# Kernel tuning notes

Hardware: AMD Instinct MI355X
Metric: run time of the kernel (lower is better)

## Reference

```python
import jax, jax.numpy as jnp
import numpy as np


def setup_inputs() -> dict:
    key = jax.random.key(0)
    k_u, k_a, k_b, k_c, k_d = jax.random.split(key, 5)
    B, T, Din, Dout, S = 16, 4096, 256, 256, 256
    return {
        "u": jax.random.normal(k_u, (B, T, Din), dtype=jnp.float32),
        "a_raw": jnp.zeros((S,), dtype=jnp.float32),
        "b": jax.random.normal(k_b, (S, Din), dtype=jnp.float32) * 0.1,
        "c": jax.random.normal(k_c, (Dout, S), dtype=jnp.float32) * 0.1,
        "d": jax.random.normal(k_d, (Dout, Din), dtype=jnp.float32) * 0.1,
    }


def reference(u, a_raw, b, c, d):
    # u: (B, T, Din) -> y: (B, T, Dout)
    # Recurrence: x_t = a * x_{t-1} + b @ u_t ;  y_t = c @ x_t + d @ u_t
    a = jnp.tanh(a_raw)                                  # (S,)
    Bu = jnp.einsum('btd,sd->bts', u, b)                 # input projection, (B,T,S)

    def step(x, bu_t):
        x = x * a + bu_t                                 # diagonal state update
        return x, x

    x0 = jnp.zeros((u.shape[0], a.shape[0]), dtype=u.dtype)
    _, xs = jax.lax.scan(step, x0, jnp.swapaxes(Bu, 0, 1))  # xs: (T,B,S)
    xs = jnp.swapaxes(xs, 0, 1)                              # (B,T,S)

    y = jnp.einsum('bts,os->bto', xs, c) + jnp.einsum('bti,oi->bto', u, d)
    return y  # dropout(p=0.0) is identity
```

## Files before the change

kernel.cpp:

```cpp
#include <hip/hip_runtime.h>

#define DEV __device__ __forceinline__

typedef unsigned short u16;
typedef __attribute__((ext_vector_type(8))) __bf16 bf16x8;
typedef __attribute__((ext_vector_type(4))) float f32x4;
typedef __attribute__((ext_vector_type(8))) unsigned short u16x8;

DEV u16 f2bf(float f) {
  unsigned u = __builtin_bit_cast(unsigned, f);
  u += 0x7fffu + ((u >> 16) & 1u);
  return (u16)(u >> 16);
}
DEV float bf2f(u16 h) {
  unsigned u = ((unsigned)h) << 16;
  return __builtin_bit_cast(float, u);
}

DEV void gl_lds16(const void* gp, void* lp) {
  __builtin_amdgcn_global_load_lds(
      (__attribute__((address_space(1))) void*)(void*)gp,
      (__attribute__((address_space(3))) void*)lp, 16, 0, 0);
}

__global__ __launch_bounds__(256) void prep_k(const float* __restrict__ a_raw,
                                              const float* __restrict__ b,
                                              const float* __restrict__ c,
                                              const float* __restrict__ d,
                                              float* __restrict__ af,
                                              u16* __restrict__ bw,
                                              u16* __restrict__ cw,
                                              u16* __restrict__ dw) {
  int i = blockIdx.x * 256 + threadIdx.x;
  if (i < 256) af[i] = tanhf(a_raw[i]);
  bw[i] = f2bf(b[i]);
  cw[i] = f2bf(c[i]);
  dw[i] = f2bf(d[i]);
}

__global__ __launch_bounds__(256) void convu_k(const float* __restrict__ u,
                                               u16* __restrict__ ub) {
  size_t i = ((size_t)blockIdx.x * 256 + threadIdx.x) * 8;
  float4 v0 = *reinterpret_cast<const float4*>(u + i);
  float4 v1 = *reinterpret_cast<const float4*>(u + i + 4);
  u16x8 o;
  o[0] = f2bf(v0.x); o[1] = f2bf(v0.y); o[2] = f2bf(v0.z); o[3] = f2bf(v0.w);
  o[4] = f2bf(v1.x); o[5] = f2bf(v1.y); o[6] = f2bf(v1.z); o[7] = f2bf(v1.w);
  *reinterpret_cast<u16x8*>(ub + i) = o;
}

__global__ __launch_bounds__(256) void gemm1_k(const u16* __restrict__ ubf,
                                               const u16* __restrict__ bw,
                                               const float* __restrict__ af,
                                               u16* __restrict__ bu,
                                               float* __restrict__ carry4) {
  __shared__ u16 As[2 * 128 * 64];
  __shared__ u16 Bs[2 * 128 * 64];
  const int tid = threadIdx.x;
  const int lane = tid & 63;
  const int wid = tid >> 6;
  const int wm = wid >> 1, wn = wid & 1;
  const int panel = blockIdx.x;
  const size_t row0 = (size_t)blockIdx.y * 128;
  const int col0 = panel * 128;

  const int rstg = tid >> 3;
  const int c16 = tid & 7;

  const f32x4 zero = {0.f, 0.f, 0.f, 0.f};
  f32x4 acc[4][4];
#pragma unroll
  for (int i = 0; i < 4; ++i)
#pragma unroll
    for (int j = 0; j < 4; ++j) acc[i][j] = zero;

#define G1_STAGE(ktv, bufv)                                                  \
  {                                                                          \
    const int kb_ = (ktv) * 64;                                              \
    _Pragma("unroll") for (int j = 0; j < 4; ++j) {                          \
      int row = j * 32 + rstg;                                               \
      int sc = c16 ^ (row & 7);                                              \
      gl_lds16(ubf + (row0 + row) * 256 + kb_ + sc * 8,                      \
               (char*)As + (bufv)*16384 + j * 4096 + wid * 1024);            \
      gl_lds16(bw + (size_t)(col0 + row) * 256 + kb_ + sc * 8,               \
               (char*)Bs + (bufv)*16384 + j * 4096 + wid * 1024);            \
    }                                                                        \
  }

  G1_STAGE(0, 0);
  __syncthreads();

#pragma unroll
  for (int kt = 0; kt < 4; ++kt) {
    const int cur = kt & 1;
    if (kt < 3) G1_STAGE(kt + 1, cur ^ 1);
    const u16* Ab = As + cur * 8192;
    const u16* Bb = Bs + cur * 8192;
#pragma unroll
    for (int kk = 0; kk < 2; ++kk) {
      const int ks = kk * 4 + (lane >> 4);
      bf16x8 afr[4], bfr[4];
#pragma unroll
      for (int mi = 0; mi < 4; ++mi) {
        int ar = wm * 64 + mi * 16 + (lane & 15);
        afr[mi] = *reinterpret_cast<const bf16x8*>(&Ab[ar * 64 + (ks ^ (ar & 7)) * 8]);
      }
#pragma unroll
      for (int ni = 0; ni < 4; ++ni) {
        int br = wn * 64 + ni * 16 + (lane & 15);
        bfr[ni] = *reinterpret_cast<const bf16x8*>(&Bb[br * 64 + (ks ^ (br & 7)) * 8]);
      }
#pragma unroll
      for (int mi = 0; mi < 4; ++mi)
#pragma unroll
        for (int ni = 0; ni < 4; ++ni)
          acc[mi][ni] = __builtin_amdgcn_mfma_f32_16x16x32_bf16(
              afr[mi], bfr[ni], acc[mi][ni], 0, 0, 0);
    }
    if (kt < 3) __syncthreads();
  }

  const size_t t2 = (size_t)blockIdx.y * 2 + wm;
#pragma unroll
  for (int mi = 0; mi < 4; ++mi) {
    int rbase = mi * 16 + (lane >> 4) * 4;
#pragma unroll
    for (int ni = 0; ni < 4; ++ni) {
      int col = col0 + wn * 64 + ni * 16 + (lane & 15);
      int colpart = (col >> 6) * 4096 + (col & 7);
      int sl = (col >> 3) & 7;
#pragma unroll
      for (int q = 0; q < 4; ++q) {
        int r = rbase + q;
        bu[t2 * 16384 + colpart + r * 64 + ((sl ^ (r & 7)) * 8)] = f2bf(acc[mi][ni][q]);
      }
    }
  }

  {
    const int tb = (lane >> 4) * 4;
#pragma unroll
    for (int ni = 0; ni < 4; ++ni) {
      int col = col0 + wn * 64 + ni * 16 + (lane & 15);
      float a = af[col];
      float c2 = a * a, c4 = c2 * c2, c8 = c4 * c4, a12 = c8 * c4;
      float base = (tb == 0) ? a12 : (tb == 4) ? c8 : (tb == 8) ? c4 : 1.0f;
#pragma unroll
      for (int mi = 0; mi < 4; ++mi) {
        float p = base, sq = 0.f;
#pragma unroll
        for (int q = 3; q >= 0; --q) {
          sq = fmaf(p, acc[mi][ni][q], sq);
          if (q) p *= a;
        }
        sq += __shfl_xor(sq, 16, 64);
        sq += __shfl_xor(sq, 32, 64);
        if ((lane >> 4) == 0) carry4[t2 * 1024 + mi * 256 + col] = sq;
      }
    }
  }
}

__global__ __launch_bounds__(256) void scan2_k(const float* __restrict__ carry4,
                                               const float* __restrict__ af,
                                               float* __restrict__ initb4) {
  int b = blockIdx.x;
  int s = threadIdx.x;
  float a = af[s];
  float a16 = a * a; a16 = a16 * a16; a16 = a16 * a16; a16 = a16 * a16;
  float x = 0.f;
  size_t base = (size_t)b * 64 * 1024 + s;
  float c0 = carry4[base], c1 = carry4[base + 256],
        c2 = carry4[base + 512], c3 = carry4[base + 768];
  for (int k = 0; k < 64; ++k) {
    size_t idx = base + (size_t)k * 1024;
    float n0 = 0.f, n1 = 0.f, n2 = 0.f, n3 = 0.f;
    if (k < 63) {
      size_t nx = idx + 1024;
      n0 = carry4[nx]; n1 = carry4[nx + 256]; n2 = carry4[nx + 512]; n3 = carry4[nx + 768];
    }
    initb4[idx] = x;        x = fmaf(a16, x, c0);
    initb4[idx + 256] = x;  x = fmaf(a16, x, c1);
    initb4[idx + 512] = x;  x = fmaf(a16, x, c2);
    initb4[idx + 768] = x;  x = fmaf(a16, x, c3);
    c0 = n0; c1 = n1; c2 = n2; c3 = n3;
  }
}

__global__ __launch_bounds__(512, 4) void gemm2_k(const u16* __restrict__ bu,
                                                  const u16* __restrict__ cw,
                                                  const u16* __restrict__ dw,
                                                  const u16* __restrict__ ubf,
                                                  const float* __restrict__ af,
                                                  const float* __restrict__ initb4,
                                                  float* __restrict__ y) {
  __shared__ u16 XS[64 * 256];
  __shared__ u16 CS[2 * 128 * 64];
  const int tid = threadIdx.x;
  const int lane = tid & 63;
  const int wid = tid >> 6;
  const int wr = wid >> 2, wc = wid & 3;
  const int by = blockIdx.y;
  const int col0 = blockIdx.x * 128;

#define G2_CS_STAGE(Wp, kbv, bufv)                                           \
  {                                                                          \
    _Pragma("unroll") for (int rr = 0; rr < 2; ++rr) {                       \
      int brow = rr * 64 + (tid >> 3);                                       \
      int sc = (tid & 7) ^ (brow & 7);                                       \
      gl_lds16((Wp) + (size_t)(col0 + brow) * 256 + (kbv) + sc * 8,          \
               (char*)CS + (bufv)*16384 + rr * 8192 + wid * 1024);           \
    }                                                                        \
  }

  const char* src = (const char*)bu + (size_t)by * 32768;
#pragma unroll
  for (int j = 0; j < 4; ++j)
    gl_lds16(src + j * 8192 + tid * 16, (char*)XS + j * 8192 + wid * 1024);
  G2_CS_STAGE(cw, 0, 0);
  __syncthreads();

  G2_CS_STAGE(cw, 64, 1);

  {
    const int s = tid & 255;
    const int pair = tid >> 8;
    const float a = af[s];
    const int colpart = (s >> 6) * 4096 + (s & 7);
    const int sl = (s >> 3) & 7;
    float x1 = initb4[(size_t)by * 1024 + (pair * 2) * 256 + s];
    float x2 = initb4[(size_t)by * 1024 + (pair * 2 + 1) * 256 + s];
#define SEG(xv, rb0)                                                          \
  {                                                                           \
    float v[8];                                                               \
    _Pragma("unroll") for (int t = 0; t < 8; ++t) {                           \
      int r = (rb0) + t;                                                      \
      v[t] = bf2f(XS[colpart + r * 64 + ((sl ^ (r & 7)) * 8)]);               \
    }                                                                         \
    _Pragma("unroll") for (int t = 0; t < 8; ++t) {                           \
      xv = fmaf(a, xv, v[t]); v[t] = xv;                                      \
    }                                                                         \
    _Pragma("unroll") for (int t = 0; t < 8; ++t) {                           \
      int r = (rb0) + t;                                                      \
      XS[colpart + r * 64 + ((sl ^ (r & 7)) * 8)] = f2bf(v[t]);               \
    }                                                                         \
  }
    SEG(x1, pair * 32 + 0);
    SEG(x1, pair * 32 + 8);
    SEG(x2, pair * 32 + 16);
    SEG(x2, pair * 32 + 24);
#undef SEG
  }
  __syncthreads();

  f32x4 acc[2][2];
  const f32x4 zero = {0.f, 0.f, 0.f, 0.f};
  acc[0][0] = zero; acc[0][1] = zero; acc[1][0] = zero; acc[1][1] = zero;

#pragma unroll
  for (int kt8 = 0; kt8 < 8; ++kt8) {
    if (kt8 >= 1 && kt8 <= 4) {
      int qq = kt8 - 1;
      int r = tid >> 3, cs = tid & 7;
      gl_lds16(ubf + ((size_t)by * 64 + r) * 256 + qq * 64 + ((cs ^ (r & 7)) * 8),
               (char*)XS + qq * 8192 + wid * 1024);
    }
    if (kt8 < 7) {
      if (kt8 + 1 < 4) G2_CS_STAGE(cw, (kt8 + 1) * 64, (kt8 + 1) & 1)
      else             G2_CS_STAGE(dw, (kt8 - 3) * 64, (kt8 + 1) & 1)
    }
    const u16* CSb = CS + (kt8 & 1) * 8192;
    const u16* XSq = XS + (kt8 & 3) * 4096;
#pragma unroll
    for (int kk = 0; kk < 2; ++kk) {
      const int ksl = kk * 4 + (lane >> 4);
      bf16x8 afr[2], bfr[2];
#pragma unroll
      for (int mi = 0; mi < 2; ++mi) {
        int ar = wr * 32 + mi * 16 + (lane & 15);
        afr[mi] = *reinterpret_cast<const bf16x8*>(&XSq[ar * 64 + ((ksl ^ (ar & 7)) * 8)]);
      }
#pragma unroll
      for (int ni = 0; ni < 2; ++ni) {
        int nr = wc * 32 + ni * 16 + (lane & 15);
        bfr[ni] = *reinterpret_cast<const bf16x8*>(&CSb[nr * 64 + ((ksl ^ (nr & 7)) * 8)]);
      }
#pragma unroll
      for (int mi = 0; mi < 2; ++mi)
#pragma unroll
        for (int ni = 0; ni < 2; ++ni)
          acc[mi][ni] = __builtin_amdgcn_mfma_f32_16x16x32_bf16(
              afr[mi], bfr[ni], acc[mi][ni], 0, 0, 0);
    }
    if (kt8 < 7) __syncthreads();
  }

#pragma unroll
  for (int mi = 0; mi < 2; ++mi) {
    int rlb = wr * 32 + mi * 16 + (lane >> 4) * 4;
#pragma unroll
    for (int ni = 0; ni < 2; ++ni) {
      int col = col0 + wc * 32 + ni * 16 + (lane & 15);
#pragma unroll
      for (int q = 0; q < 4; ++q)
        y[((size_t)by * 64 + rlb + q) * 256 + col] = acc[mi][ni][q];
    }
  }
}

extern "C" void kernel_launch(void* const* d_in, const int* in_sizes, int n_in,
                              void* d_out, int out_size, void* d_ws, size_t ws_size,
                              hipStream_t stream) {
  const float* u = (const float*)d_in[0];
  const float* a_raw = (const float*)d_in[1];
  const float* b = (const float*)d_in[2];
  const float* c = (const float*)d_in[3];
  const float* d = (const float*)d_in[4];
  float* y = (float*)d_out;
  char* ws = (char*)d_ws;

  const size_t MB = 1u << 20;
  float* af = (float*)(ws);
  u16* bw = (u16*)(ws + 4096);
  u16* cw = (u16*)(ws + 4096 + 131072);
  u16* dw = (u16*)(ws + 4096 + 2 * 131072);
  u16* ubf = (u16*)(ws + 1 * MB);
  u16* bu = (u16*)(ws + 33 * MB);
  float* carry4 = (float*)(ws + 65 * MB);
  float* initb4 = (float*)(ws + 69 * MB);

  prep_k<<<256, 256, 0, stream>>>(a_raw, b, c, d, af, bw, cw, dw);
  convu_k<<<8192, 256, 0, stream>>>(u, ubf);
  gemm1_k<<<dim3(2, 512), 256, 0, stream>>>(ubf, bw, af, bu, carry4);
  scan2_k<<<16, 256, 0, stream>>>(carry4, af, initb4);
  gemm2_k<<<dim3(2, 1024), 512, 0, stream>>>(bu, cw, dw, ubf, af, initb4, y);
}
```

Before: 100.5 us.

## Fuse u conversion into gemm1 and precompute D·u alongside B·u

The separate fp32-to-bf16 conversion kernel for u is removed; gemm1 now loads fp32 u directly, converts it in registers and computes both B·u and D·u in one pass over a concatenated 512-row weight block. D·u is stored as bf16 and loaded by gemm2 as the initial accumulator, so gemm2 runs only the C·x half of its K loop and no longer reads u. This cuts one kernel launch and a full pass over u, at the cost of an extra bf16 rounding of D·u, a larger gemm1 tile with more register pressure, and gemm1 losing its double-buffered LDS staging.

```diff
diff --git a/kernel.cpp b/kernel.cpp
--- a/kernel.cpp
+++ b/kernel.cpp
@@ -21,6 +21,13 @@
   __builtin_amdgcn_global_load_lds(
       (__attribute__((address_space(1))) void*)(void*)gp,
       (__attribute__((address_space(3))) void*)lp, 16, 0, 0);
+}
+
+DEV u16x8 pack8(float4 a, float4 b) {
+  u16x8 o;
+  o[0] = f2bf(a.x); o[1] = f2bf(a.y); o[2] = f2bf(a.z); o[3] = f2bf(a.w);
+  o[4] = f2bf(b.x); o[5] = f2bf(b.y); o[6] = f2bf(b.z); o[7] = f2bf(b.w);
+  return o;
 }
 
 __global__ __launch_bounds__(256) void prep_k(const float* __restrict__ a_raw,
@@ -28,120 +35,108 @@
                                               const float* __restrict__ c,
                                               const float* __restrict__ d,
                                               float* __restrict__ af,
-                                              u16* __restrict__ bw,
-                                              u16* __restrict__ cw,
-                                              u16* __restrict__ dw) {
+                                              u16* __restrict__ wq,
+                                              u16* __restrict__ cw) {
   int i = blockIdx.x * 256 + threadIdx.x;
   if (i < 256) af[i] = tanhf(a_raw[i]);
-  bw[i] = f2bf(b[i]);
+  wq[i] = f2bf(b[i]);
+  wq[65536 + i] = f2bf(d[i]);
   cw[i] = f2bf(c[i]);
-  dw[i] = f2bf(d[i]);
-}
-
-__global__ __launch_bounds__(256) void convu_k(const float* __restrict__ u,
-                                               u16* __restrict__ ub) {
-  size_t i = ((size_t)blockIdx.x * 256 + threadIdx.x) * 8;
-  float4 v0 = *reinterpret_cast<const float4*>(u + i);
-  float4 v1 = *reinterpret_cast<const float4*>(u + i + 4);
-  u16x8 o;
-  o[0] = f2bf(v0.x); o[1] = f2bf(v0.y); o[2] = f2bf(v0.z); o[3] = f2bf(v0.w);
-  o[4] = f2bf(v1.x); o[5] = f2bf(v1.y); o[6] = f2bf(v1.z); o[7] = f2bf(v1.w);
-  *reinterpret_cast<u16x8*>(ub + i) = o;
-}
-
-__global__ __launch_bounds__(256) void gemm1_k(const u16* __restrict__ ubf,
-                                               const u16* __restrict__ bw,
-                                               const float* __restrict__ af,
-                                               u16* __restrict__ bu,
-                                               float* __restrict__ carry4) {
-  __shared__ u16 As[2 * 128 * 64];
-  __shared__ u16 Bs[2 * 128 * 64];
+}
+
+__global__ __launch_bounds__(512, 2) void gemm1_k(const float* __restrict__ u,
+                                                  const u16* __restrict__ wq,
+                                                  const float* __restrict__ af,
+                                                  u16* __restrict__ bu,
+                                                  u16* __restrict__ ud,
+                                                  float* __restrict__ carry4) {
+  __shared__ u16 As[128 * 64];
+  __shared__ u16 Bs[512 * 64];
   const int tid = threadIdx.x;
   const int lane = tid & 63;
   const int wid = tid >> 6;
-  const int wm = wid >> 1, wn = wid & 1;
-  const int panel = blockIdx.x;
-  const size_t row0 = (size_t)blockIdx.y * 128;
-  const int col0 = panel * 128;
-
-  const int rstg = tid >> 3;
-  const int c16 = tid & 7;
-
+  const int wr = wid >> 2, wc = wid & 3;
+  const size_t row0 = (size_t)blockIdx.x * 128;
+
+  const int arow = tid >> 2;
+  const int ak0 = (tid & 3) * 16;
+  const int s0 = (tid & 3) * 2;
+
+  f32x4 acc[4][8];
   const f32x4 zero = {0.f, 0.f, 0.f, 0.f};
-  f32x4 acc[4][4];
 #pragma unroll
   for (int i = 0; i < 4; ++i)
 #pragma unroll
-    for (int j = 0; j < 4; ++j) acc[i][j] = zero;
-
-#define G1_STAGE(ktv, bufv)                                                  \
-  {                                                                          \
-    const int kb_ = (ktv) * 64;                                              \
-    _Pragma("unroll") for (int j = 0; j < 4; ++j) {                          \
-      int row = j * 32 + rstg;                                               \
-      int sc = c16 ^ (row & 7);                                              \
-      gl_lds16(ubf + (row0 + row) * 256 + kb_ + sc * 8,                      \
-               (char*)As + (bufv)*16384 + j * 4096 + wid * 1024);            \
-      gl_lds16(bw + (size_t)(col0 + row) * 256 + kb_ + sc * 8,               \
-               (char*)Bs + (bufv)*16384 + j * 4096 + wid * 1024);            \
-    }                                                                        \
-  }
-
-  G1_STAGE(0, 0);
-  __syncthreads();
+    for (int j = 0; j < 8; ++j) acc[i][j] = zero;
 
 #pragma unroll
   for (int kt = 0; kt < 4; ++kt) {
-    const int cur = kt & 1;
-    if (kt < 3) G1_STAGE(kt + 1, cur ^ 1);
-    const u16* Ab = As + cur * 8192;
-    const u16* Bb = Bs + cur * 8192;
+    const int kb = kt * 64;
+    const float* up = u + (row0 + arow) * 256 + kb + ak0;
+    float4 f0 = *reinterpret_cast<const float4*>(up);
+    float4 f1 = *reinterpret_cast<const float4*>(up + 4);
+    float4 f2 = *reinterpret_cast<const float4*>(up + 8);
+    float4 f3 = *reinterpret_cast<const float4*>(up + 12);
+#pragma unroll
+    for (int r = 0; r < 8; ++r) {
+      int wrow = r * 64 + (tid >> 3);
+      int sc = (tid & 7) ^ (wrow & 7);
+      gl_lds16(wq + (size_t)wrow * 256 + kb + sc * 8,
+               (char*)Bs + r * 8192 + wid * 1024);
+    }
+    *reinterpret_cast<u16x8*>(&As[arow * 64 + ((s0) ^ (arow & 7)) * 8]) = pack8(f0, f1);
+    *reinterpret_cast<u16x8*>(&As[arow * 64 + ((s0 + 1) ^ (arow & 7)) * 8]) = pack8(f2, f3);
+    __syncthreads();
 #pragma unroll
     for (int kk = 0; kk < 2; ++kk) {
       const int ks = kk * 4 + (lane >> 4);
-      bf16x8 afr[4], bfr[4];
+      bf16x8 afr[4];
 #pragma unroll
       for (int mi = 0; mi < 4; ++mi) {
-        int ar = wm * 64 + mi * 16 + (lane & 15);
-        afr[mi] = *reinterpret_cast<const bf16x8*>(&Ab[ar * 64 + (ks ^ (ar & 7)) * 8]);
-      }
-#pragma unroll
-      for (int ni = 0; ni < 4; ++ni) {
-        int br = wn * 64 + ni * 16 + (lane & 15);
-        bfr[ni] = *reinterpret_cast<const bf16x8*>(&Bb[br * 64 + (ks ^ (br & 7)) * 8]);
-      }
-#pragma unroll
-      for (int mi = 0; mi < 4; ++mi)
-#pragma unroll
-        for (int ni = 0; ni < 4; ++ni)
-          acc[mi][ni] = __builtin_amdgcn_mfma_f32_16x16x32_bf16(
-              afr[mi], bfr[ni], acc[mi][ni], 0, 0, 0);
+        int ar = wr * 64 + mi * 16 + (lane & 15);
+        afr[mi] = *reinterpret_cast<const bf16x8*>(&As[ar * 64 + (ks ^ (ar & 7)) * 8]);
+      }
+#pragma unroll
+      for (int nh = 0; nh < 2; ++nh) {
+        bf16x8 bfr[4];
+#pragma unroll
+        for (int nj = 0; nj < 4; ++nj) {
+          int br = wc * 128 + (nh * 4 + nj) * 16 + (lane & 15);
+          bfr[nj] = *reinterpret_cast<const bf16x8*>(&Bs[br * 64 + (ks ^ (br & 7)) * 8]);
+        }
+#pragma unroll
+        for (int mi = 0; mi < 4; ++mi)
+#pragma unroll
+          for (int nj = 0; nj < 4; ++nj)
+            acc[mi][nh * 4 + nj] = __builtin_amdgcn_mfma_f32_16x16x32_bf16(
+                afr[mi], bfr[nj], acc[mi][nh * 4 + nj], 0, 0, 0);
+      }
     }
     if (kt < 3) __syncthreads();
   }
 
-  const size_t t2 = (size_t)blockIdx.y * 2 + wm;
-#pragma unroll
-  for (int mi = 0; mi < 4; ++mi) {
-    int rbase = mi * 16 + (lane >> 4) * 4;
-#pragma unroll
-    for (int ni = 0; ni < 4; ++ni) {
-      int col = col0 + wn * 64 + ni * 16 + (lane & 15);
-      int colpart = (col >> 6) * 4096 + (col & 7);
-      int sl = (col >> 3) & 7;
-#pragma unroll
-      for (int q = 0; q < 4; ++q) {
-        int r = rbase + q;
-        bu[t2 * 16384 + colpart + r * 64 + ((sl ^ (r & 7)) * 8)] = f2bf(acc[mi][ni][q]);
-      }
-    }
-  }
-
-  {
+  const size_t t2 = (size_t)blockIdx.x * 2 + wr;
+
+  if (wc < 2) {
+#pragma unroll
+    for (int mi = 0; mi < 4; ++mi) {
+      int rbase = mi * 16 + (lane >> 4) * 4;
+#pragma unroll
+      for (int ni = 0; ni < 8; ++ni) {
+        int col = wc * 128 + ni * 16 + (lane & 15);
+        int colpart = (col >> 6) * 4096 + (col & 7);
+        int sl = (col >> 3) & 7;
+#pragma unroll
+        for (int q = 0; q < 4; ++q) {
+          int r = rbase + q;
+          bu[t2 * 16384 + colpart + r * 64 + ((sl ^ (r & 7)) * 8)] = f2bf(acc[mi][ni][q]);
+        }
+      }
+    }
     const int tb = (lane >> 4) * 4;
 #pragma unroll
-    for (int ni = 0; ni < 4; ++ni) {
-      int col = col0 + wn * 64 + ni * 16 + (lane & 15);
+    for (int ni = 0; ni < 8; ++ni) {
+      int col = wc * 128 + ni * 16 + (lane & 15);
       float a = af[col];
       float c2 = a * a, c4 = c2 * c2, c8 = c4 * c4, a12 = c8 * c4;
       float base = (tb == 0) ? a12 : (tb == 4) ? c8 : (tb == 8) ? c4 : 1.0f;
@@ -156,6 +151,18 @@
         sq += __shfl_xor(sq, 16, 64);
         sq += __shfl_xor(sq, 32, 64);
         if ((lane >> 4) == 0) carry4[t2 * 1024 + mi * 256 + col] = sq;
+      }
+    }
+  } else {
+#pragma unroll
+    for (int mi = 0; mi < 4; ++mi) {
+      int rbase = mi * 16 + (lane >> 4) * 4;
+#pragma unroll
+      for (int ni = 0; ni < 8; ++ni) {
+        int cold = (wc - 2) * 128 + ni * 16 + (lane & 15);
+#pragma unroll
+        for (int q = 0; q < 4; ++q)
+          ud[(t2 * 64 + rbase + q) * 256 + cold] = f2bf(acc[mi][ni][q]);
       }
     }
   }
@@ -189,8 +196,7 @@
 
 __global__ __launch_bounds__(512, 4) void gemm2_k(const u16* __restrict__ bu,
                                                   const u16* __restrict__ cw,
-                                                  const u16* __restrict__ dw,
-                                                  const u16* __restrict__ ubf,
+                                                  const u16* __restrict__ ud,
                                                   const float* __restrict__ af,
                                                   const float* __restrict__ initb4,
                                                   float* __restrict__ y) {
@@ -203,12 +209,12 @@
   const int by = blockIdx.y;
   const int col0 = blockIdx.x * 128;
 
-#define G2_CS_STAGE(Wp, kbv, bufv)                                           \
+#define G2_CS_STAGE(kbv, bufv)                                               \
   {                                                                          \
     _Pragma("unroll") for (int rr = 0; rr < 2; ++rr) {                       \
       int brow = rr * 64 + (tid >> 3);                                       \
       int sc = (tid & 7) ^ (brow & 7);                                       \
-      gl_lds16((Wp) + (size_t)(col0 + brow) * 256 + (kbv) + sc * 8,          \
+      gl_lds16(cw + (size_t)(col0 + brow) * 256 + (kbv) + sc * 8,            \
                (char*)CS + (bufv)*16384 + rr * 8192 + wid * 1024);           \
     }                                                                        \
   }
@@ -217,10 +223,10 @@
 #pragma unroll
   for (int j = 0; j < 4; ++j)
     gl_lds16(src + j * 8192 + tid * 16, (char*)XS + j * 8192 + wid * 1024);
-  G2_CS_STAGE(cw, 0, 0);
+  G2_CS_STAGE(0, 0);
   __syncthreads();
 
-  G2_CS_STAGE(cw, 64, 1);
+  G2_CS_STAGE(64, 1);
 
   {
     const int s = tid & 255;
@@ -251,26 +257,25 @@
     SEG(x2, pair * 32 + 24);
 #undef SEG
   }
+
+  f32x4 acc[2][2];
+#pragma unroll
+  for (int mi = 0; mi < 2; ++mi) {
+    int rlb = wr * 32 + mi * 16 + (lane >> 4) * 4;
+#pragma unroll
+    for (int ni = 0; ni < 2; ++ni) {
+      int col = col0 + wc * 32 + ni * 16 + (lane & 15);
+#pragma unroll
+      for (int q = 0; q < 4; ++q)
+        acc[mi][ni][q] = bf2f(ud[((size_t)by * 64 + rlb + q) * 256 + col]);
+    }
+  }
   __syncthreads();
 
-  f32x4 acc[2][2];
-  const f32x4 zero = {0.f, 0.f, 0.f, 0.f};
-  acc[0][0] = zero; acc[0][1] = zero; acc[1][0] = zero; acc[1][1] = zero;
-
-#pragma unroll
-  for (int kt8 = 0; kt8 < 8; ++kt8) {
-    if (kt8 >= 1 && kt8 <= 4) {
-      int qq = kt8 - 1;
-      int r = tid >> 3, cs = tid & 7;
-      gl_lds16(ubf + ((size_t)by * 64 + r) * 256 + qq * 64 + ((cs ^ (r & 7)) * 8),
-               (char*)XS + qq * 8192 + wid * 1024);
-    }
-    if (kt8 < 7) {
-      if (kt8 + 1 < 4) G2_CS_STAGE(cw, (kt8 + 1) * 64, (kt8 + 1) & 1)
-      else             G2_CS_STAGE(dw, (kt8 - 3) * 64, (kt8 + 1) & 1)
-    }
-    const u16* CSb = CS + (kt8 & 1) * 8192;
-    const u16* XSq = XS + (kt8 & 3) * 4096;
+#pragma unroll
+  for (int kt = 0; kt < 4; ++kt) {
+    const u16* CSb = CS + (kt & 1) * 8192;
+    const u16* XSq = XS + kt * 4096;
 #pragma unroll
     for (int kk = 0; kk < 2; ++kk) {
       const int ksl = kk * 4 + (lane >> 4);
@@ -292,7 +297,10 @@
           acc[mi][ni] = __builtin_amdgcn_mfma_f32_16x16x32_bf16(
               afr[mi], bfr[ni], acc[mi][ni], 0, 0, 0);
     }
-    if (kt8 < 7) __syncthreads();
+    if (kt < 3) {
+      __syncthreads();
+      if (kt < 2) G2_CS_STAGE((kt + 2) * 64, kt & 1);
+    }
   }
 
 #pragma unroll
@@ -321,17 +329,15 @@
 
   const size_t MB = 1u << 20;
   float* af = (float*)(ws);
-  u16* bw = (u16*)(ws + 4096);
-  u16* cw = (u16*)(ws + 4096 + 131072);
-  u16* dw = (u16*)(ws + 4096 + 2 * 131072);
-  u16* ubf = (u16*)(ws + 1 * MB);
-  u16* bu = (u16*)(ws + 33 * MB);
+  u16* wq = (u16*)(ws + 4096);
+  u16* cw = (u16*)(ws + 4096 + 262144);
+  u16* bu = (u16*)(ws + 1 * MB);
+  u16* ud = (u16*)(ws + 33 * MB);
   float* carry4 = (float*)(ws + 65 * MB);
   float* initb4 = (float*)(ws + 69 * MB);
 
-  prep_k<<<256, 256, 0, stream>>>(a_raw, b, c, d, af, bw, cw, dw);
-  convu_k<<<8192, 256, 0, stream>>>(u, ubf);
-  gemm1_k<<<dim3(2, 512), 256, 0, stream>>>(ubf, bw, af, bu, carry4);
+  prep_k<<<256, 256, 0, stream>>>(a_raw, b, c, d, af, wq, cw);
+  gemm1_k<<<512, 512, 0, stream>>>(u, wq, af, bu, ud, carry4);
   scan2_k<<<16, 256, 0, stream>>>(carry4, af, initb4);
-  gemm2_k<<<dim3(2, 1024), 512, 0, stream>>>(bu, cw, dw, ubf, af, initb4, y);
-}
+  gemm2_k<<<dim3(2, 1024), 512, 0, stream>>>(bu, cw, ud, af, initb4, y);
+}
```

After: 115.2 us. +14.6%, slower.
